# Optimization experiments

Measured on AMD Instinct MI355X. Metric: run time of the kernel, lower is better.

Reference implementation:

```python
import jax, jax.numpy as jnp
import numpy as np
from functools import partial

VOCAB, EMB = 32000, 512
HIDDEN = (1024, 512, 256)
OUT = 7
S, T = 1024, 64  # S = scan (seq) axis, T = 'timesteps' (effective batch)


def _lstm_layer(x, Wih, Whh, bih, bhh):
    """PyTorch-semantics LSTM over axis 0. x: (S, B, E) -> hs: (S, B, H)."""
    B = x.shape[1]
    H = Whh.shape[1]
    # precompute input contribution to all gates: (S, B, 4H)
    xg = jnp.einsum('sbe,ge->sbg', x, Wih) + bih + bhh

    def step(carry, xg_t):
        h, c = carry
        gates = xg_t + h @ Whh.T  # (B, 4H)
        i, f, g, o = jnp.split(gates, 4, axis=-1)  # torch gate order i,f,g,o
        i = jax.nn.sigmoid(i)
        f = jax.nn.sigmoid(f)
        g = jnp.tanh(g)
        o = jax.nn.sigmoid(o)
        c = f * c + i * g
        h = o * jnp.tanh(c)
        return (h, c), h

    init = (jnp.zeros((B, H), x.dtype), jnp.zeros((B, H), x.dtype))
    _, hs = jax.lax.scan(step, init, xg)
    return hs


def setup_inputs():
    key = jax.random.key(0)
    ks = jax.random.split(key, 16)
    inp = {
        'tokens': jax.random.randint(ks[0], (S, T), 0, VOCAB),
        'emb': jax.random.normal(ks[1], (VOCAB, EMB), jnp.float32) * 0.02,
    }
    dims = [(EMB, HIDDEN[0]), (HIDDEN[0], HIDDEN[1]), (HIDDEN[1], HIDDEN[2])]
    for li, (e, h) in enumerate(dims):
        s = 1.0 / np.sqrt(h)
        inp[f'Wih{li}'] = jax.random.uniform(ks[2 + 4 * li], (4 * h, e), jnp.float32, -s, s)
        inp[f'Whh{li}'] = jax.random.uniform(ks[3 + 4 * li], (4 * h, h), jnp.float32, -s, s)
        inp[f'bih{li}'] = jax.random.uniform(ks[4 + 4 * li], (4 * h,), jnp.float32, -s, s)
        inp[f'bhh{li}'] = jax.random.uniform(ks[5 + 4 * li], (4 * h,), jnp.float32, -s, s)
    s = 1.0 / np.sqrt(HIDDEN[2])
    inp['Wlin'] = jax.random.uniform(ks[14], (OUT, HIDDEN[2]), jnp.float32, -s, s)
    inp['blin'] = jax.random.uniform(ks[15], (OUT,), jnp.float32, -s, s)
    return inp


def reference(tokens, emb, Wih0, Whh0, bih0, bhh0, Wih1, Whh1, bih1, bhh1,
              Wih2, Whh2, bih2, bhh2, Wlin, blin):
    x = emb[tokens]                                  # (S, T, EMB)
    h = _lstm_layer(x, Wih0, Whh0, bih0, bhh0)       # (S, T, 1024)
    h = _lstm_layer(h, Wih1, Whh1, bih1, bhh1)       # (S, T, 512)
    h = _lstm_layer(h, Wih2, Whh2, bih2, bhh2)       # (S, T, 256)
    last = h[:, T - 1, :]                            # out[:, timesteps-1, :]
    out = last @ Wlin.T + blin                       # (S, OUT); dropout is identity in eval
    return out
```

## Files before the change

### kernel.cpp

```cpp
#include <hip/hip_runtime.h>
#include <math.h>

#define SLEN 1024

__device__ __forceinline__ float sigf(float x) { return 1.0f / (1.0f + __expf(-x)); }

__device__ __forceinline__ float agent_ld(const float* p) {
  return __hip_atomic_load(p, __ATOMIC_RELAXED, __HIP_MEMORY_SCOPE_AGENT);
}
__device__ __forceinline__ void agent_st(float* p, float v) {
  __hip_atomic_store(p, v, __ATOMIC_RELAXED, __HIP_MEMORY_SCOPE_AGENT);
}
__device__ __forceinline__ bool is_sent(float f) { return __float_as_uint(f) == 0xFFFFFFFFu; }

__device__ __forceinline__ void pin4(float4& v) {
  asm volatile("" : "+v"(v.x), "+v"(v.y), "+v"(v.z), "+v"(v.w));
}
#define DOT4(acc, wv, iv)                                                  \
  acc += (wv).x * (iv).x + (wv).y * (iv).y + (wv).z * (iv).z + (wv).w * (iv).w

__global__ __launch_bounds__(512, 2) void xg0_k(const int* __restrict__ tokens,
                                                const float* __restrict__ emb,
                                                const float* __restrict__ Wih0,
                                                const float* __restrict__ bih0,
                                                const float* __restrict__ bhh0,
                                                float* __restrict__ xg0) {
  const int tid = threadIdx.x, c = tid & 63, w = tid >> 6;
  const int ublk = blockIdx.x & 127;
  const int tph  = blockIdx.x >> 7;
  const int u = ublk * 8 + w;
  const float4* emb4 = (const float4*)emb;
  float4 wr[4][2];
  float bb[4];
  #pragma unroll
  for (int g = 0; g < 4; ++g) {
    const size_t row = (size_t)g * 1024 + u;
    const float4* w4 = (const float4*)(Wih0 + row * 512);
    wr[g][0] = w4[2 * c];
    wr[g][1] = w4[2 * c + 1];
    bb[g] = bih0[row] + bhh0[row];
  }
  float4* xg4 = (float4*)xg0;
  for (int t = tph; t < SLEN; t += 8) {
    const int tok = tokens[t * 64 + 63];
    const float4 e0 = emb4[(size_t)tok * 128 + 2 * c];
    const float4 e1 = emb4[(size_t)tok * 128 + 2 * c + 1];
    float a[4] = {0.f, 0.f, 0.f, 0.f};
    #pragma unroll
    for (int g = 0; g < 4; ++g) { DOT4(a[g], wr[g][0], e0); DOT4(a[g], wr[g][1], e1); }
    #pragma unroll
    for (int off = 32; off > 0; off >>= 1)
      #pragma unroll
      for (int g = 0; g < 4; ++g) a[g] += __shfl_xor(a[g], off);
    if (c == 0)
      xg4[(size_t)t * 1024 + u] =
          make_float4(a[0] + bb[0], a[1] + bb[1], a[2] + bb[2], a[3] + bb[3]);
  }
}

__device__ void l0_role(int ublk, char* blob, const float* __restrict__ Whh,
                        const float* __restrict__ xg0, float* __restrict__ hout) {
  float* in_base = (float*)blob;
  float* hg = in_base + 2 * 1024;
  const int tid = threadIdx.x, c = tid & 63, w = tid >> 6;
  const int u0 = ublk * 8, u = u0 + w;

  float4 wreg[4][4];
  #pragma unroll
  for (int g = 0; g < 4; ++g) {
    const float4* whh4 = (const float4*)(Whh + ((size_t)g * 1024 + u) * 1024);
    #pragma unroll
    for (int s = 0; s < 4; ++s) wreg[g][s] = whh4[s * 64 + c];
  }
  const float4* xg4 = (const float4*)xg0;
  float cst = 0.f;

  for (int t = 0; t < SLEN; ++t) {
    #pragma unroll
    for (int g = 0; g < 4; ++g)
      #pragma unroll
      for (int s = 0; s < 4; ++s) pin4(wreg[g][s]);

    float4 xgv = make_float4(0.f, 0.f, 0.f, 0.f);
    if (c == 0) xgv = xg4[(size_t)t * 1024 + u];

    float hv0 = 0.f, hv1 = 0.f;
    if (t > 0) {
      const float* hsrc = hout + (size_t)(t - 1) * 1024 + 2 * tid;
      for (;;) {
        hv0 = agent_ld(hsrc);
        hv1 = agent_ld(hsrc + 1);
        if (!is_sent(hv0) && !is_sent(hv1)) break;
      }
    }
    float* dst = in_base + (t & 1) * 1024;
    dst[2 * tid] = hv0;
    dst[2 * tid + 1] = hv1;
    __syncthreads();

    float a[4] = {0.f, 0.f, 0.f, 0.f};
    const float4* iv4 = (const float4*)dst;
    #pragma unroll
    for (int s = 0; s < 4; ++s) {
      const float4 iv = iv4[s * 64 + c];
      #pragma unroll
      for (int g = 0; g < 4; ++g) DOT4(a[g], wreg[g][s], iv);
    }
    #pragma unroll
    for (int off = 32; off > 0; off >>= 1)
      #pragma unroll
      for (int g = 0; g < 4; ++g) a[g] += __shfl_xor(a[g], off);

    if (c == 0) {
      const float I = sigf(a[0] + xgv.x);
      const float F = sigf(a[1] + xgv.y);
      const float G = tanhf(a[2] + xgv.z);
      const float O = sigf(a[3] + xgv.w);
      cst = F * cst + I * G;
      hg[w] = O * tanhf(cst);
    }
    __syncthreads();
    if (tid < 8) agent_st(hout + (size_t)t * 1024 + u0 + tid, hg[tid]);
  }
}

template<int HOUT, int EIN, int RSLOTS>
__device__ void lstm_role(int ublk, char* blob,
                          const float* __restrict__ Wih, const float* __restrict__ Whh,
                          const float* __restrict__ bih, const float* __restrict__ bhh,
                          const float* __restrict__ in_hist, float* __restrict__ hout) {
  constexpr int C      = EIN + HOUT;
  constexpr int SLOTS  = C / 256;
  constexpr int LSLOTS = SLOTS - RSLOTS;
  constexpr int XQ     = EIN / 4;
  constexpr int EPN    = EIN / 512;
  constexpr bool HGUARD = (HOUT < 512);

  float4* wlds4  = (float4*)blob;
  float* in_base = (float*)blob + (size_t)LSLOTS * 32 * 64 * 4;
  float* hg      = in_base + 2 * C;

  const int tid = threadIdx.x, c = tid & 63, w = tid >> 6;
  const int u0 = ublk * 8, u = u0 + w;

  for (int k = tid; k < LSLOTS * 32 * 64; k += 512) {
    const int cc = k & 63, rr = k >> 6, r = rr & 31, sl = rr >> 5;
    const int g = r & 3, wu = r >> 2;
    const size_t grow = (size_t)g * HOUT + (size_t)(u0 + wu);
    const float4* wih4 = (const float4*)(Wih + grow * EIN);
    const float4* whh4 = (const float4*)(Whh + grow * HOUT);
    const int c4 = (RSLOTS + sl) * 64 + cc;
    wlds4[k] = (c4 < XQ) ? wih4[c4] : whh4[c4 - XQ];
  }

  float4 wreg[4][RSLOTS];
  #pragma unroll
  for (int g = 0; g < 4; ++g) {
    const size_t grow = (size_t)g * HOUT + (size_t)u;
    const float4* wih4 = (const float4*)(Wih + grow * EIN);
    const float4* whh4 = (const float4*)(Whh + grow * HOUT);
    #pragma unroll
    for (int s = 0; s < RSLOTS; ++s) {
      const int c4 = s * 64 + c;
      wreg[g][s] = (c4 < XQ) ? wih4[c4] : whh4[c4 - XQ];
    }
  }
  float bg[4] = {0.f, 0.f, 0.f, 0.f};
  float cst = 0.f;
  if (c == 0) {
    #pragma unroll
    for (int g = 0; g < 4; ++g) bg[g] = bih[g * HOUT + u] + bhh[g * HOUT + u];
  }

  for (int t = 0; t < SLEN; ++t) {
    #pragma unroll
    for (int g = 0; g < 4; ++g)
      #pragma unroll
      for (int s = 0; s < RSLOTS; ++s) pin4(wreg[g][s]);

    float ev[EPN];
    float hv = 0.f;
    const float* esrc = in_hist + (size_t)t * EIN + EPN * tid;
    const float* hsrc = hout + (size_t)((t > 0 ? t : 1) - 1) * HOUT + tid;
    const bool hon   = (!HGUARD) || (tid < HOUT);
    const bool hneed = (t > 0) && hon;

    for (;;) {
      bool ok = true;
      #pragma unroll
      for (int i = 0; i < EPN; ++i) ev[i] = agent_ld(esrc + i);
      if (hneed) { hv = agent_ld(hsrc); ok &= !is_sent(hv); }
      #pragma unroll
      for (int i = 0; i < EPN; ++i) ok &= !is_sent(ev[i]);
      if (ok) break;
    }
    if (!hneed) hv = 0.f;

    float* dst = in_base + (t & 1) * C;
    #pragma unroll
    for (int i = 0; i < EPN; ++i) dst[EPN * tid + i] = ev[i];
    if (hon) dst[EIN + tid] = hv;
    __syncthreads();

    float a[4] = {0.f, 0.f, 0.f, 0.f};
    const float4* iv4 = (const float4*)dst;
    #pragma unroll
    for (int s = 0; s < RSLOTS; ++s) {
      const float4 iv = iv4[s * 64 + c];
      #pragma unroll
      for (int g = 0; g < 4; ++g) DOT4(a[g], wreg[g][s], iv);
    }
    #pragma unroll
    for (int sl = 0; sl < LSLOTS; ++sl) {
      const float4 iv = iv4[(RSLOTS + sl) * 64 + c];
      #pragma unroll
      for (int g = 0; g < 4; ++g) {
        const float4 wv = wlds4[((sl * 32) + (w * 4 + g)) * 64 + c];
        DOT4(a[g], wv, iv);
      }
    }
    #pragma unroll
    for (int off = 32; off > 0; off >>= 1)
      #pragma unroll
      for (int g = 0; g < 4; ++g) a[g] += __shfl_xor(a[g], off);

    if (c == 0) {
      const float I = sigf(a[0] + bg[0]);
      const float F = sigf(a[1] + bg[1]);
      const float G = tanhf(a[2] + bg[2]);
      const float O = sigf(a[3] + bg[3]);
      cst = F * cst + I * G;
      hg[w] = O * tanhf(cst);
    }
    __syncthreads();
    if (tid < 8) agent_st(hout + (size_t)t * HOUT + u0 + tid, hg[tid]);
  }
}

__device__ void final_role(int fb, const float* __restrict__ h2,
                           const float* __restrict__ Wlin, const float* __restrict__ blin,
                           float* __restrict__ out) {
  const int tid = threadIdx.x;
  float wl[7];
  #pragma unroll
  for (int o = 0; o < 7; ++o) wl[o] = 0.f;
  if (tid < 256) {
    #pragma unroll
    for (int o = 0; o < 7; ++o) wl[o] = Wlin[o * 256 + tid];
  }
  __shared__ float red[4][7];
  for (int t = fb; t < SLEN; t += 8) {
    float h = 0.0f;
    if (tid < 256) {
      h = agent_ld(h2 + (size_t)t * 256 + tid);
      while (is_sent(h)) h = agent_ld(h2 + (size_t)t * 256 + tid);
    }
    float p[7];
    #pragma unroll
    for (int o = 0; o < 7; ++o) p[o] = h * wl[o];
    #pragma unroll
    for (int off = 32; off > 0; off >>= 1) {
      #pragma unroll
      for (int o = 0; o < 7; ++o) p[o] += __shfl_xor(p[o], off);
    }
    const int w = tid >> 6;
    if (w < 4 && (tid & 63) == 0) {
      #pragma unroll
      for (int o = 0; o < 7; ++o) red[w][o] = p[o];
    }
    __syncthreads();
    if (tid == 0) {
      #pragma unroll
      for (int o = 0; o < 7; ++o)
        out[t * 7 + o] = red[0][o] + red[1][o] + red[2][o] + red[3][o] + blin[o];
    }
    __syncthreads();
  }
}

#define PIPE_DYN_LDS 110624

__global__ __attribute__((amdgpu_flat_work_group_size(512, 512),
                          amdgpu_waves_per_eu(2, 2))) void pipe_k(
    const float* __restrict__ xg0,
    const float* __restrict__ Whh0,
    const float* __restrict__ Wih1, const float* __restrict__ Whh1,
    const float* __restrict__ bih1, const float* __restrict__ bhh1,
    const float* __restrict__ Wih2, const float* __restrict__ Whh2,
    const float* __restrict__ bih2, const float* __restrict__ bhh2,
    const float* __restrict__ Wlin, const float* __restrict__ blin,
    float* __restrict__ h0, float* __restrict__ h1, float* __restrict__ h2,
    float* __restrict__ out) {
  extern __shared__ float4 dyn4[];
  char* blob = (char*)dyn4;
  const int b = blockIdx.x;
  if (b < 128) {
    l0_role(b, blob, Whh0, xg0, h0);
  } else if (b < 192) {
    lstm_role<512, 1024, 3>(b - 128, blob, Wih1, Whh1, bih1, bhh1, h0, h1);
  } else if (b < 224) {
    lstm_role<256, 512, 3>(b - 192, blob, Wih2, Whh2, bih2, bhh2, h1, h2);
  } else {
    final_role(b - 224, h2, Wlin, blin, out);
  }
}

extern "C" void kernel_launch(void* const* d_in, const int* in_sizes, int n_in,
                              void* d_out, int out_size, void* d_ws, size_t ws_size,
                              hipStream_t stream) {
  const int*   tokens = (const int*)  d_in[0];
  const float* emb  = (const float*)d_in[1];
  const float* Wih0 = (const float*)d_in[2];
  const float* Whh0 = (const float*)d_in[3];
  const float* bih0 = (const float*)d_in[4];
  const float* bhh0 = (const float*)d_in[5];
  const float* Wih1 = (const float*)d_in[6];
  const float* Whh1 = (const float*)d_in[7];
  const float* bih1 = (const float*)d_in[8];
  const float* bhh1 = (const float*)d_in[9];
  const float* Wih2 = (const float*)d_in[10];
  const float* Whh2 = (const float*)d_in[11];
  const float* bih2 = (const float*)d_in[12];
  const float* bhh2 = (const float*)d_in[13];
  const float* Wlin = (const float*)d_in[14];
  const float* blin = (const float*)d_in[15];

  float* xg0 = (float*)d_ws;
  float* h0  = xg0 + (size_t)1024 * 4096;
  float* h1  = h0 + (size_t)1024 * 1024;
  float* h2  = h1 + (size_t)1024 * 512;

  (void)hipFuncSetAttribute((const void*)pipe_k,
                            hipFuncAttributeMaxDynamicSharedMemorySize,
                            PIPE_DYN_LDS);

  hipMemsetAsync(h0, 0xFF,
                 ((size_t)1024 * 1024 + (size_t)1024 * 512 + (size_t)1024 * 256) *
                     sizeof(float),
                 stream);
  xg0_k<<<1024, 512, 0, stream>>>(tokens, emb, Wih0, bih0, bhh0, xg0);
  pipe_k<<<232, 512, PIPE_DYN_LDS, stream>>>(xg0, Whh0,
                                             Wih1, Whh1, bih1, bhh1,
                                             Wih2, Whh2, bih2, bhh2,
                                             Wlin, blin, h0, h1, h2, (float*)d_out);
}
```

Before: 2.947 ms.

## Pack inter-layer hidden states as bf16 pairs and halve layer-0 block count

Layer-0 and layer-1 hidden states are exchanged between blocks as packed bf16 pairs, which halves the words polled and stored per step. Each layer-0 block now computes 16 units, with half its weights held in LDS, so layer 0 needs 64 blocks instead of 128 and fewer blocks take part in cross-block synchronisation. Polling moves to a single wave with s_sleep backoff, and the grid shrinks from 232 to 168 blocks. Rounding the recurrent activations to bf16 loses precision that can compound over 1024 steps, and layer 0 does more LDS traffic per step.

```diff
diff --git a/kernel.cpp b/kernel.cpp
--- a/kernel.cpp
+++ b/kernel.cpp
@@ -1,17 +1,33 @@
 #include <hip/hip_runtime.h>
 #include <math.h>
+#include <stdint.h>
 
 #define SLEN 1024
 
 __device__ __forceinline__ float sigf(float x) { return 1.0f / (1.0f + __expf(-x)); }
 
-__device__ __forceinline__ float agent_ld(const float* p) {
+__device__ __forceinline__ uint32_t aldu(const uint32_t* p) {
   return __hip_atomic_load(p, __ATOMIC_RELAXED, __HIP_MEMORY_SCOPE_AGENT);
 }
-__device__ __forceinline__ void agent_st(float* p, float v) {
+__device__ __forceinline__ void astu(uint32_t* p, uint32_t v) {
   __hip_atomic_store(p, v, __ATOMIC_RELAXED, __HIP_MEMORY_SCOPE_AGENT);
 }
-__device__ __forceinline__ bool is_sent(float f) { return __float_as_uint(f) == 0xFFFFFFFFu; }
+__device__ __forceinline__ float aldf(const float* p) {
+  return __hip_atomic_load(p, __ATOMIC_RELAXED, __HIP_MEMORY_SCOPE_AGENT);
+}
+__device__ __forceinline__ void astf(float* p, float v) {
+  __hip_atomic_store(p, v, __ATOMIC_RELAXED, __HIP_MEMORY_SCOPE_AGENT);
+}
+__device__ __forceinline__ bool sentu(uint32_t v) { return v == 0xFFFFFFFFu; }
+__device__ __forceinline__ bool sentf(float f) { return __float_as_uint(f) == 0xFFFFFFFFu; }
+__device__ __forceinline__ float blo(uint32_t d) { return __uint_as_float(d << 16); }
+__device__ __forceinline__ float bhi(uint32_t d) { return __uint_as_float(d & 0xFFFF0000u); }
+__device__ __forceinline__ uint32_t bpack(float lo, float hi) {
+  uint32_t a = __float_as_uint(lo), b = __float_as_uint(hi);
+  a = (a + 0x7FFFu + ((a >> 16) & 1u)) >> 16;
+  b = (b + 0x7FFFu + ((b >> 16) & 1u)) & 0xFFFF0000u;
+  return b | a;
+}
 
 __device__ __forceinline__ void pin4(float4& v) {
   asm volatile("" : "+v"(v.x), "+v"(v.y), "+v"(v.z), "+v"(v.w));
@@ -58,87 +74,114 @@
   }
 }
 
-__device__ void l0_role(int ublk, char* blob, const float* __restrict__ Whh,
-                        const float* __restrict__ xg0, float* __restrict__ hout) {
-  float* in_base = (float*)blob;
-  float* hg = in_base + 2 * 1024;
+__device__ void l0_role(int blk, char* blob, const float* __restrict__ Whh,
+                        const float* __restrict__ xg0, uint32_t* __restrict__ houtp) {
+  float4* wlds4 = (float4*)blob;
+  float*  in_f  = (float*)(blob + 131072);
+  float*  hg    = in_f + 1024;
   const int tid = threadIdx.x, c = tid & 63, w = tid >> 6;
-  const int u0 = ublk * 8, u = u0 + w;
-
+  const int u0 = blk * 16;
+
+  for (int k = tid; k < 8192; k += 512) {
+    const int wg = k >> 8, rem = k & 255, s = rem >> 6, cc = rem & 63;
+    const int ww = wg >> 2, g = wg & 3;
+    wlds4[k] = ((const float4*)Whh)[((size_t)g * 1024 + (u0 + 8 + ww)) * 256 + s * 64 + cc];
+  }
   float4 wreg[4][4];
   #pragma unroll
   for (int g = 0; g < 4; ++g) {
-    const float4* whh4 = (const float4*)(Whh + ((size_t)g * 1024 + u) * 1024);
-    #pragma unroll
-    for (int s = 0; s < 4; ++s) wreg[g][s] = whh4[s * 64 + c];
-  }
+    const float4* r4 = (const float4*)Whh + ((size_t)g * 1024 + (u0 + w)) * 256;
+    #pragma unroll
+    for (int s = 0; s < 4; ++s) wreg[g][s] = r4[s * 64 + c];
+  }
+  __syncthreads();
+
   const float4* xg4 = (const float4*)xg0;
   float cst = 0.f;
 
   for (int t = 0; t < SLEN; ++t) {
     #pragma unroll
-    for (int g = 0; g < 4; ++g)
+    for (int g = 0; g < 4; ++g) {
       #pragma unroll
       for (int s = 0; s < 4; ++s) pin4(wreg[g][s]);
-
-    float4 xgv = make_float4(0.f, 0.f, 0.f, 0.f);
-    if (c == 0) xgv = xg4[(size_t)t * 1024 + u];
-
-    float hv0 = 0.f, hv1 = 0.f;
-    if (t > 0) {
-      const float* hsrc = hout + (size_t)(t - 1) * 1024 + 2 * tid;
-      for (;;) {
-        hv0 = agent_ld(hsrc);
-        hv1 = agent_ld(hsrc + 1);
-        if (!is_sent(hv0) && !is_sent(hv1)) break;
-      }
-    }
-    float* dst = in_base + (t & 1) * 1024;
-    dst[2 * tid] = hv0;
-    dst[2 * tid + 1] = hv1;
-    __syncthreads();
-
-    float a[4] = {0.f, 0.f, 0.f, 0.f};
-    const float4* iv4 = (const float4*)dst;
+    }
+
+    if (w == 0) {
+      if (t > 0) {
+        const uint32_t* hp = houtp + (size_t)(t - 1) * 512;
+        uint32_t hv[8];
+        for (;;) {
+          bool ok = true;
+          #pragma unroll
+          for (int i = 0; i < 8; ++i) hv[i] = aldu(hp + i * 64 + c);
+          #pragma unroll
+          for (int i = 0; i < 8; ++i) ok &= !sentu(hv[i]);
+          if (ok) break;
+          __builtin_amdgcn_s_sleep(2);
+        }
+        #pragma unroll
+        for (int i = 0; i < 8; ++i)
+          ((float2*)in_f)[i * 64 + c] = make_float2(blo(hv[i]), bhi(hv[i]));
+      } else {
+        #pragma unroll
+        for (int i = 0; i < 8; ++i)
+          ((float2*)in_f)[i * 64 + c] = make_float2(0.f, 0.f);
+      }
+    }
+    __syncthreads();
+
+    float a[8];
+    #pragma unroll
+    for (int r = 0; r < 8; ++r) a[r] = 0.f;
+    const float4* iv4 = (const float4*)in_f;
     #pragma unroll
     for (int s = 0; s < 4; ++s) {
       const float4 iv = iv4[s * 64 + c];
       #pragma unroll
-      for (int g = 0; g < 4; ++g) DOT4(a[g], wreg[g][s], iv);
+      for (int g = 0; g < 4; ++g) {
+        DOT4(a[g], wreg[g][s], iv);
+        const float4 wv = wlds4[(w * 4 + g) * 256 + s * 64 + c];
+        DOT4(a[4 + g], wv, iv);
+      }
     }
     #pragma unroll
     for (int off = 32; off > 0; off >>= 1)
       #pragma unroll
-      for (int g = 0; g < 4; ++g) a[g] += __shfl_xor(a[g], off);
-
-    if (c == 0) {
-      const float I = sigf(a[0] + xgv.x);
-      const float F = sigf(a[1] + xgv.y);
-      const float G = tanhf(a[2] + xgv.z);
-      const float O = sigf(a[3] + xgv.w);
+      for (int r = 0; r < 8; ++r) a[r] += __shfl_xor(a[r], off);
+
+    if (c < 2) {
+      const int lu = (c == 0) ? w : 8 + w;
+      const int base = c * 4;
+      const float4 xgv = xg4[(size_t)t * 1024 + u0 + lu];
+      const float I = sigf(a[base + 0] + xgv.x);
+      const float F = sigf(a[base + 1] + xgv.y);
+      const float G = tanhf(a[base + 2] + xgv.z);
+      const float O = sigf(a[base + 3] + xgv.w);
       cst = F * cst + I * G;
-      hg[w] = O * tanhf(cst);
-    }
-    __syncthreads();
-    if (tid < 8) agent_st(hout + (size_t)t * 1024 + u0 + tid, hg[tid]);
-  }
-}
-
-template<int HOUT, int EIN, int RSLOTS>
+      hg[lu] = O * tanhf(cst);
+    }
+    __syncthreads();
+    if (tid < 8)
+      astu(houtp + (size_t)t * 512 + blk * 8 + tid, bpack(hg[2 * tid], hg[2 * tid + 1]));
+  }
+}
+
+template<int HOUT, int EIN, int RSLOTS, bool PACK_OUT>
 __device__ void lstm_role(int ublk, char* blob,
                           const float* __restrict__ Wih, const float* __restrict__ Whh,
                           const float* __restrict__ bih, const float* __restrict__ bhh,
-                          const float* __restrict__ in_hist, float* __restrict__ hout) {
-  constexpr int C      = EIN + HOUT;
-  constexpr int SLOTS  = C / 256;
+                          const uint32_t* __restrict__ inp,
+                          uint32_t* __restrict__ houtp, float* __restrict__ houtf) {
+  constexpr int C = EIN + HOUT;
+  constexpr int SLOTS = C / 256;
   constexpr int LSLOTS = SLOTS - RSLOTS;
-  constexpr int XQ     = EIN / 4;
-  constexpr int EPN    = EIN / 512;
-  constexpr bool HGUARD = (HOUT < 512);
-
-  float4* wlds4  = (float4*)blob;
-  float* in_base = (float*)blob + (size_t)LSLOTS * 32 * 64 * 4;
-  float* hg      = in_base + 2 * C;
+  constexpr int XQ = EIN / 4;
+  constexpr int AND = EIN / 128;
+  constexpr int BND = PACK_OUT ? (HOUT / 128) : (HOUT / 64);
+
+  float4* wlds4 = (float4*)blob;
+  float*  in_f  = (float*)(blob + (size_t)LSLOTS * 32 * 64 * 16);
+  float*  hg    = in_f + C;
 
   const int tid = threadIdx.x, c = tid & 63, w = tid >> 6;
   const int u0 = ublk * 8, u = u0 + w;
@@ -152,7 +195,6 @@
     const int c4 = (RSLOTS + sl) * 64 + cc;
     wlds4[k] = (c4 < XQ) ? wih4[c4] : whh4[c4 - XQ];
   }
-
   float4 wreg[4][RSLOTS];
   #pragma unroll
   for (int g = 0; g < 4; ++g) {
@@ -171,39 +213,70 @@
     #pragma unroll
     for (int g = 0; g < 4; ++g) bg[g] = bih[g * HOUT + u] + bhh[g * HOUT + u];
   }
+  __syncthreads();
 
   for (int t = 0; t < SLEN; ++t) {
     #pragma unroll
-    for (int g = 0; g < 4; ++g)
+    for (int g = 0; g < 4; ++g) {
       #pragma unroll
       for (int s = 0; s < RSLOTS; ++s) pin4(wreg[g][s]);
-
-    float ev[EPN];
-    float hv = 0.f;
-    const float* esrc = in_hist + (size_t)t * EIN + EPN * tid;
-    const float* hsrc = hout + (size_t)((t > 0 ? t : 1) - 1) * HOUT + tid;
-    const bool hon   = (!HGUARD) || (tid < HOUT);
-    const bool hneed = (t > 0) && hon;
-
-    for (;;) {
-      bool ok = true;
-      #pragma unroll
-      for (int i = 0; i < EPN; ++i) ev[i] = agent_ld(esrc + i);
-      if (hneed) { hv = agent_ld(hsrc); ok &= !is_sent(hv); }
-      #pragma unroll
-      for (int i = 0; i < EPN; ++i) ok &= !is_sent(ev[i]);
-      if (ok) break;
-    }
-    if (!hneed) hv = 0.f;
-
-    float* dst = in_base + (t & 1) * C;
-    #pragma unroll
-    for (int i = 0; i < EPN; ++i) dst[EPN * tid + i] = ev[i];
-    if (hon) dst[EIN + tid] = hv;
+    }
+
+    if (w == 0) {
+      uint32_t av[AND];
+      float bf[BND];
+      uint32_t bu[BND];
+      for (;;) {
+        bool ok = true;
+        #pragma unroll
+        for (int i = 0; i < AND; ++i) av[i] = aldu(inp + (size_t)t * (EIN / 2) + i * 64 + c);
+        if (t > 0) {
+          if constexpr (PACK_OUT) {
+            #pragma unroll
+            for (int i = 0; i < BND; ++i)
+              bu[i] = aldu(houtp + (size_t)(t - 1) * (HOUT / 2) + i * 64 + c);
+            #pragma unroll
+            for (int i = 0; i < BND; ++i) ok &= !sentu(bu[i]);
+          } else {
+            #pragma unroll
+            for (int i = 0; i < BND; ++i)
+              bf[i] = aldf(houtf + (size_t)(t - 1) * HOUT + i * 64 + c);
+            #pragma unroll
+            for (int i = 0; i < BND; ++i) ok &= !sentf(bf[i]);
+          }
+        }
+        #pragma unroll
+        for (int i = 0; i < AND; ++i) ok &= !sentu(av[i]);
+        if (ok) break;
+        __builtin_amdgcn_s_sleep(2);
+      }
+      #pragma unroll
+      for (int i = 0; i < AND; ++i)
+        ((float2*)in_f)[i * 64 + c] = make_float2(blo(av[i]), bhi(av[i]));
+      if (t > 0) {
+        if constexpr (PACK_OUT) {
+          #pragma unroll
+          for (int i = 0; i < BND; ++i)
+            ((float2*)(in_f + EIN))[i * 64 + c] = make_float2(blo(bu[i]), bhi(bu[i]));
+        } else {
+          #pragma unroll
+          for (int i = 0; i < BND; ++i) in_f[EIN + i * 64 + c] = bf[i];
+        }
+      } else {
+        if constexpr (PACK_OUT) {
+          #pragma unroll
+          for (int i = 0; i < BND; ++i)
+            ((float2*)(in_f + EIN))[i * 64 + c] = make_float2(0.f, 0.f);
+        } else {
+          #pragma unroll
+          for (int i = 0; i < BND; ++i) in_f[EIN + i * 64 + c] = 0.f;
+        }
+      }
+    }
     __syncthreads();
 
     float a[4] = {0.f, 0.f, 0.f, 0.f};
-    const float4* iv4 = (const float4*)dst;
+    const float4* iv4 = (const float4*)in_f;
     #pragma unroll
     for (int s = 0; s < RSLOTS; ++s) {
       const float4 iv = iv4[s * 64 + c];
@@ -233,13 +306,21 @@
       hg[w] = O * tanhf(cst);
     }
     __syncthreads();
-    if (tid < 8) agent_st(hout + (size_t)t * HOUT + u0 + tid, hg[tid]);
-  }
-}
-
-__device__ void final_role(int fb, const float* __restrict__ h2,
+    if constexpr (PACK_OUT) {
+      if (tid < 4)
+        astu(houtp + (size_t)t * (HOUT / 2) + ublk * 4 + tid,
+             bpack(hg[2 * tid], hg[2 * tid + 1]));
+    } else {
+      if (tid < 8)
+        astf(houtf + (size_t)t * HOUT + ublk * 8 + tid, hg[tid]);
+    }
+  }
+}
+
+__device__ void final_role(int fb, char* blob, const float* __restrict__ h2f,
                            const float* __restrict__ Wlin, const float* __restrict__ blin,
                            float* __restrict__ out) {
+  float* red = (float*)blob;
   const int tid = threadIdx.x;
   float wl[7];
   #pragma unroll
@@ -248,12 +329,14 @@
     #pragma unroll
     for (int o = 0; o < 7; ++o) wl[o] = Wlin[o * 256 + tid];
   }
-  __shared__ float red[4][7];
   for (int t = fb; t < SLEN; t += 8) {
-    float h = 0.0f;
+    float h = 0.f;
     if (tid < 256) {
-      h = agent_ld(h2 + (size_t)t * 256 + tid);
-      while (is_sent(h)) h = agent_ld(h2 + (size_t)t * 256 + tid);
+      h = aldf(h2f + (size_t)t * 256 + tid);
+      while (sentf(h)) {
+        __builtin_amdgcn_s_sleep(2);
+        h = aldf(h2f + (size_t)t * 256 + tid);
+      }
     }
     float p[7];
     #pragma unroll
@@ -266,42 +349,40 @@
     const int w = tid >> 6;
     if (w < 4 && (tid & 63) == 0) {
       #pragma unroll
-      for (int o = 0; o < 7; ++o) red[w][o] = p[o];
+      for (int o = 0; o < 7; ++o) red[w * 7 + o] = p[o];
     }
     __syncthreads();
     if (tid == 0) {
       #pragma unroll
       for (int o = 0; o < 7; ++o)
-        out[t * 7 + o] = red[0][o] + red[1][o] + red[2][o] + red[3][o] + blin[o];
-    }
-    __syncthreads();
-  }
-}
-
-#define PIPE_DYN_LDS 110624
+        out[t * 7 + o] = red[0 + o] + red[7 + o] + red[14 + o] + red[21 + o] + blin[o];
+    }
+    __syncthreads();
+  }
+}
+
+#define PIPE_DYN_LDS 135232
 
 __global__ __attribute__((amdgpu_flat_work_group_size(512, 512),
                           amdgpu_waves_per_eu(2, 2))) void pipe_k(
-    const float* __restrict__ xg0,
-    const float* __restrict__ Whh0,
+    const float* __restrict__ xg0, const float* __restrict__ Whh0,
     const float* __restrict__ Wih1, const float* __restrict__ Whh1,
     const float* __restrict__ bih1, const float* __restrict__ bhh1,
     const float* __restrict__ Wih2, const float* __restrict__ Whh2,
     const float* __restrict__ bih2, const float* __restrict__ bhh2,
     const float* __restrict__ Wlin, const float* __restrict__ blin,
-    float* __restrict__ h0, float* __restrict__ h1, float* __restrict__ h2,
+    uint32_t* __restrict__ h0p, uint32_t* __restrict__ h1p, float* __restrict__ h2f,
     float* __restrict__ out) {
-  extern __shared__ float4 dyn4[];
-  char* blob = (char*)dyn4;
+  extern __shared__ __align__(16) char blob[];
   const int b = blockIdx.x;
-  if (b < 128) {
-    l0_role(b, blob, Whh0, xg0, h0);
-  } else if (b < 192) {
-    lstm_role<512, 1024, 3>(b - 128, blob, Wih1, Whh1, bih1, bhh1, h0, h1);
-  } else if (b < 224) {
-    lstm_role<256, 512, 3>(b - 192, blob, Wih2, Whh2, bih2, bhh2, h1, h2);
+  if (b < 64) {
+    l0_role(b, blob, Whh0, xg0, h0p);
+  } else if (b < 128) {
+    lstm_role<512, 1024, 3, true>(b - 64, blob, Wih1, Whh1, bih1, bhh1, h0p, h1p, nullptr);
+  } else if (b < 160) {
+    lstm_role<256, 512, 3, false>(b - 128, blob, Wih2, Whh2, bih2, bhh2, h1p, nullptr, h2f);
   } else {
-    final_role(b - 224, h2, Wlin, blin, out);
+    final_role(b - 160, blob, h2f, Wlin, blin, out);
   }
 }
 
@@ -325,22 +406,21 @@
   const float* Wlin = (const float*)d_in[14];
   const float* blin = (const float*)d_in[15];
 
-  float* xg0 = (float*)d_ws;
-  float* h0  = xg0 + (size_t)1024 * 4096;
-  float* h1  = h0 + (size_t)1024 * 1024;
-  float* h2  = h1 + (size_t)1024 * 512;
+  float*    xg0 = (float*)d_ws;
+  uint32_t* h0p = (uint32_t*)(xg0 + (size_t)1024 * 4096);
+  uint32_t* h1p = h0p + (size_t)1024 * 512;
+  float*    h2f = (float*)(h1p + (size_t)1024 * 256);
 
   (void)hipFuncSetAttribute((const void*)pipe_k,
                             hipFuncAttributeMaxDynamicSharedMemorySize,
                             PIPE_DYN_LDS);
 
-  hipMemsetAsync(h0, 0xFF,
-                 ((size_t)1024 * 1024 + (size_t)1024 * 512 + (size_t)1024 * 256) *
-                     sizeof(float),
+  hipMemsetAsync(h0p, 0xFF,
+                 ((size_t)1024 * 512 + (size_t)1024 * 256 + (size_t)1024 * 256) * 4,
                  stream);
   xg0_k<<<1024, 512, 0, stream>>>(tokens, emb, Wih0, bih0, bhh0, xg0);
-  pipe_k<<<232, 512, PIPE_DYN_LDS, stream>>>(xg0, Whh0,
+  pipe_k<<<168, 512, PIPE_DYN_LDS, stream>>>(xg0, Whh0,
                                              Wih1, Whh1, bih1, bhh1,
                                              Wih2, Whh2, bih2, bhh2,
-                                             Wlin, blin, h0, h1, h2, (float*)d_out);
-}
+                                             Wlin, blin, h0p, h1p, h2f, (float*)d_out);
+}
```

Result: slower. 4.384 ms (+48.7%).
